# Kernel tuning notes

Measured on AMD Instinct MI355X. Metric: run time of the kernel, lower is better.

Reference implementation:

```python
import jax, jax.numpy as jnp
import numpy as np

EMBED_DIM = 256
UNITS = 512


def setup_inputs() -> dict:
    key = jax.random.key(0)
    k1, k2, k3, k4, k5, k6, k7, k8 = jax.random.split(key, 8)
    B, L = 2048, 64
    features = jax.random.normal(k1, (B, L, EMBED_DIM), dtype=jnp.float32)
    hidden = jax.random.normal(k2, (B, UNITS), dtype=jnp.float32)
    s1 = 1.0 / np.sqrt(EMBED_DIM)
    s2 = 1.0 / np.sqrt(UNITS)
    W1 = jax.random.normal(k3, (EMBED_DIM, UNITS), dtype=jnp.float32) * s1
    b1 = jnp.zeros((UNITS,), dtype=jnp.float32)
    W2 = jax.random.normal(k4, (UNITS, UNITS), dtype=jnp.float32) * s2
    b2 = jnp.zeros((UNITS,), dtype=jnp.float32)
    V = jax.random.normal(k5, (UNITS, 1), dtype=jnp.float32) * s2
    bV = jnp.zeros((1,), dtype=jnp.float32)
    return {"features": features, "hidden": hidden, "W1": W1, "b1": b1,
            "W2": W2, "b2": b2, "V": V, "bV": bV}


def reference(features, hidden, W1, b1, W2, b2, V, bV):
    # features: [B, L, D_feat]; hidden: [B, U]
    # score = tanh(W1(features) + W2(hidden)[:, None])  -> [B, L, U]
    proj_f = jnp.einsum('bld,du->blu', features, W1) + b1
    proj_h = hidden @ W2 + b2                         # [B, U]
    score = jnp.tanh(proj_f + proj_h[:, None, :])     # [B, L, U]
    logits = jnp.einsum('blu,uo->blo', score, V) + bV  # [B, L, 1]
    attention_weights = jax.nn.softmax(logits, axis=1)  # softmax over L
    context_vector = jnp.sum(attention_weights * features, axis=1)  # [B, D_feat]
    return context_vector, attention_weights
```

## Files before the change

### kernel.cpp

```cpp
#include <hip/hip_runtime.h>
#include <math.h>

#define B_N 2048
#define L_N 64
#define D_N 256
#define U_N 512
#define NB  4

typedef __attribute__((ext_vector_type(8))) short bf16x8;
typedef __attribute__((ext_vector_type(4))) float f32x4;

__device__ __forceinline__ float fast_tanh(float x) {
    float e = __builtin_amdgcn_exp2f(x * 2.8853900817779268f);
    float r = __builtin_amdgcn_rcpf(e + 1.0f);
    return fmaf(-2.0f, r, 1.0f);
}
__device__ __forceinline__ ushort f2bf(float x) {
    uint b = __float_as_uint(x);
    uint r = (b + 0x7FFF + ((b >> 16) & 1)) >> 16;
    return (ushort)r;
}
__device__ __forceinline__ float bf2f(ushort u) {
    uint v = ((uint)u) << 16;
    return __uint_as_float(v);
}

__global__ __launch_bounds__(256) void pack_weights(
    const float* __restrict__ W1, const float* __restrict__ W2,
    ushort* __restrict__ W1p, ushort* __restrict__ W2p)
{
    ushort tmp[8];
    if (blockIdx.x < 64) {
        int g = blockIdx.x * 256 + threadIdx.x;
        int ntg = g >> 9, ks = (g >> 6) & 7, lane = g & 63;
        int n  = ntg * 16 + (lane & 15);
        int kb = ks * 32 + (lane >> 4) * 8;
#pragma unroll
        for (int j = 0; j < 8; ++j) tmp[j] = f2bf(W1[(kb + j) * U_N + n]);
        *(uint4*)&W1p[(size_t)g * 8] = *(uint4*)tmp;
    } else {
        int g = (blockIdx.x - 64) * 256 + threadIdx.x;
        int ntg = g >> 10, ks = (g >> 6) & 15, lane = g & 63;
        int n  = ntg * 16 + (lane & 15);
        int kb = ks * 32 + (lane >> 4) * 8;
#pragma unroll
        for (int j = 0; j < 8; ++j) tmp[j] = f2bf(W2[(kb + j) * U_N + n]);
        *(uint4*)&W2p[(size_t)g * 8] = *(uint4*)tmp;
    }
}

__global__ __launch_bounds__(256) void proj_h_mfma(
    const float* __restrict__ hidden, const ushort* __restrict__ W2p,
    const float* __restrict__ b1, const float* __restrict__ b2,
    ushort* __restrict__ ph)
{
    __shared__ ushort As[16 * 512];

    const int t  = threadIdx.x;
    const int b0 = blockIdx.x * 16;
    const int u0 = blockIdx.y * 128;

#pragma unroll
    for (int i = 0; i < 4; ++i) {
        int f = t + i * 256;
        int m = f >> 6, c = f & 63;
        float4 x0 = *(const float4*)&hidden[(b0 + m) * U_N + c * 8];
        float4 x1 = *(const float4*)&hidden[(b0 + m) * U_N + c * 8 + 4];
        ushort tmp[8] = {f2bf(x0.x), f2bf(x0.y), f2bf(x0.z), f2bf(x0.w),
                         f2bf(x1.x), f2bf(x1.y), f2bf(x1.z), f2bf(x1.w)};
        *(uint4*)&As[(m * 64 + (c ^ (m & 7))) * 8] = *(uint4*)tmp;
    }
    __syncthreads();

    const int w = t >> 6, lane = t & 63;
    const int ml = lane & 15, q = lane >> 4;

    f32x4 acc[2];
#pragma unroll
    for (int nt = 0; nt < 2; ++nt) acc[nt] = (f32x4){0.f, 0.f, 0.f, 0.f};

    for (int ks = 0; ks < 16; ++ks) {
        int c = ks * 4 + q;
        bf16x8 a = *(const bf16x8*)&As[(ml * 64 + (c ^ (ml & 7))) * 8];
        bf16x8 bb[2];
#pragma unroll
        for (int nt = 0; nt < 2; ++nt) {
            int ntg = blockIdx.y * 8 + w * 2 + nt;
            bb[nt] = *(const bf16x8*)&W2p[(size_t)((ntg * 16 + ks) * 64 + lane) * 8];
        }
#pragma unroll
        for (int nt = 0; nt < 2; ++nt)
            acc[nt] = __builtin_amdgcn_mfma_f32_16x16x32_bf16(a, bb[nt], acc[nt], 0, 0, 0);
    }

#pragma unroll
    for (int nt = 0; nt < 2; ++nt) {
        int n = u0 + (w * 2 + nt) * 16 + ml;
        float bias = b1[n] + b2[n];
#pragma unroll
        for (int r = 0; r < 4; ++r)
            ph[(size_t)(b0 + q * 4 + r) * U_N + n] = f2bf(acc[nt][r] + bias);
    }
}

__global__ __launch_bounds__(256, 2) void attn_kernel(
    const float* __restrict__ features, const ushort* __restrict__ W1p,
    const float* __restrict__ V, const float* __restrict__ bV,
    const ushort* __restrict__ ph, float* __restrict__ out)
{
    __shared__ ushort As[2][64 * 256];
    __shared__ float lpart[4][64];
    __shared__ float wls[64];

    const int t    = threadIdx.x;
    const int w    = t >> 6;
    const int lane = t & 63;
    const int ml   = lane & 15;
    const int q    = lane >> 4;
    const int b0   = blockIdx.x * NB;

    float4 pf[16];

#define ISSUE(bb) do {                                                        \
        const float* fb_ = features + (size_t)(bb) * (L_N * D_N);             \
        _Pragma("unroll")                                                     \
        for (int i = 0; i < 8; ++i) {                                         \
            int f_ = t + i * 256;                                             \
            int m_ = f_ >> 5, c_ = f_ & 31;                                   \
            pf[2*i]   = *(const float4*)&fb_[m_ * D_N + c_ * 8];              \
            pf[2*i+1] = *(const float4*)&fb_[m_ * D_N + c_ * 8 + 4];          \
        }                                                                     \
    } while (0)

#define WRITE(buf) do {                                                       \
        _Pragma("unroll")                                                     \
        for (int i = 0; i < 8; ++i) {                                         \
            int f_ = t + i * 256;                                             \
            int m_ = f_ >> 5, c_ = f_ & 31;                                   \
            float4 x0_ = pf[2*i], x1_ = pf[2*i+1];                            \
            ushort tmp_[8] = {f2bf(x0_.x), f2bf(x0_.y), f2bf(x0_.z), f2bf(x0_.w), \
                              f2bf(x1_.x), f2bf(x1_.y), f2bf(x1_.z), f2bf(x1_.w)}; \
            *(uint4*)&As[buf][(m_ * 32 + (c_ ^ (m_ & 31))) * 8] = *(uint4*)tmp_;  \
        }                                                                     \
    } while (0)

    ISSUE(b0);
    WRITE(0);
    __syncthreads();

    const ushort* W1w = W1p + (size_t)(w * 8) * 8 * 64 * 8;
    int cur = 0;

    for (int bi = 0; bi < NB; ++bi) {
        const int b = b0 + bi;

        if (bi + 1 < NB) ISSUE(b + 1);
        __builtin_amdgcn_sched_barrier(0);

        float lp[16];
#pragma unroll
        for (int j = 0; j < 16; ++j) lp[j] = 0.f;

        for (int uc = 0; uc < 4; ++uc) {
            f32x4 acc[4][2];
#pragma unroll
            for (int mt = 0; mt < 4; ++mt)
#pragma unroll
                for (int nt = 0; nt < 2; ++nt)
                    acc[mt][nt] = (f32x4){0.f, 0.f, 0.f, 0.f};

            bf16x8 bf0[2], bf1[2], bfn[2];
#pragma unroll
            for (int nt = 0; nt < 2; ++nt) {
                bf0[nt] = *(const bf16x8*)&W1w[(size_t)(((uc * 2 + nt) * 8 + 0) * 64 + lane) * 8];
                bf1[nt] = *(const bf16x8*)&W1w[(size_t)(((uc * 2 + nt) * 8 + 1) * 64 + lane) * 8];
            }

            for (int ks = 0; ks < 8; ++ks) {
                if (ks < 6) {
#pragma unroll
                    for (int nt = 0; nt < 2; ++nt)
                        bfn[nt] = *(const bf16x8*)&W1w[(size_t)(((uc * 2 + nt) * 8 + ks + 2) * 64 + lane) * 8];
                }
                bf16x8 a[4];
#pragma unroll
                for (int mt = 0; mt < 4; ++mt) {
                    int m = mt * 16 + ml;
                    int c = ks * 4 + q;
                    a[mt] = *(const bf16x8*)&As[cur][(m * 32 + (c ^ (m & 31))) * 8];
                }
#pragma unroll
                for (int nt = 0; nt < 2; ++nt)
#pragma unroll
                    for (int mt = 0; mt < 4; ++mt)
                        acc[mt][nt] = __builtin_amdgcn_mfma_f32_16x16x32_bf16(
                            a[mt], bf0[nt], acc[mt][nt], 0, 0, 0);
                bf0[0] = bf1[0]; bf0[1] = bf1[1];
                bf1[0] = bfn[0]; bf1[1] = bfn[1];
            }

#pragma unroll
            for (int nt = 0; nt < 2; ++nt) {
                int n = w * 128 + uc * 32 + nt * 16 + ml;
                float phv = bf2f(ph[(size_t)b * U_N + n]);
                float vv  = V[n];
#pragma unroll
                for (int mt = 0; mt < 4; ++mt)
#pragma unroll
                    for (int r = 0; r < 4; ++r) {
                        float s = fast_tanh(acc[mt][nt][r] + phv);
                        lp[mt * 4 + r] = fmaf(s, vv, lp[mt * 4 + r]);
                    }
            }
        }

#pragma unroll
        for (int off = 1; off <= 8; off <<= 1)
#pragma unroll
            for (int j = 0; j < 16; ++j)
                lp[j] += __shfl_xor(lp[j], off);

        __syncthreads();
        if (bi + 1 < NB) WRITE(cur ^ 1);

        if (ml == 0) {
#pragma unroll
            for (int mt = 0; mt < 4; ++mt)
#pragma unroll
                for (int r = 0; r < 4; ++r)
                    lpart[w][mt * 16 + q * 4 + r] = lp[mt * 4 + r];
        }
        __syncthreads();

        if (t < 64) {
            float lsum = bV[0] + lpart[0][t] + lpart[1][t] + lpart[2][t] + lpart[3][t];
            float mx = lsum;
#pragma unroll
            for (int off = 32; off > 0; off >>= 1)
                mx = fmaxf(mx, __shfl_xor(mx, off));
            float e = __expf(lsum - mx);
            float ssum = e;
#pragma unroll
            for (int off = 32; off > 0; off >>= 1)
                ssum += __shfl_xor(ssum, off);
            float wt = e / ssum;
            wls[t] = wt;
            out[(size_t)B_N * D_N + (size_t)b * L_N + t] = wt;
        }
        __syncthreads();

        float ctx = 0.f;
#pragma unroll 16
        for (int l = 0; l < L_N; ++l) {
            ushort u = As[cur][(l * 32 + ((t >> 3) ^ (l & 31))) * 8 + (t & 7)];
            ctx = fmaf(wls[l], bf2f(u), ctx);
        }
        out[(size_t)b * D_N + t] = ctx;

        cur ^= 1;
    }
#undef ISSUE
#undef WRITE
}

extern "C" void kernel_launch(void* const* d_in, const int* in_sizes, int n_in,
                              void* d_out, int out_size, void* d_ws, size_t ws_size,
                              hipStream_t stream) {
    const float* features = (const float*)d_in[0];
    const float* hidden   = (const float*)d_in[1];
    const float* W1       = (const float*)d_in[2];
    const float* b1       = (const float*)d_in[3];
    const float* W2       = (const float*)d_in[4];
    const float* b2       = (const float*)d_in[5];
    const float* V        = (const float*)d_in[6];
    const float* bV       = (const float*)d_in[7];
    float* out = (float*)d_out;

    ushort* ph  = (ushort*)d_ws;
    ushort* W1p = (ushort*)((char*)d_ws + (size_t)B_N * U_N * 2);
    ushort* W2p = (ushort*)((char*)d_ws + (size_t)B_N * U_N * 2 + (size_t)D_N * U_N * 2);

    pack_weights<<<192, 256, 0, stream>>>(W1, W2, W1p, W2p);
    proj_h_mfma<<<dim3(B_N / 16, U_N / 128), 256, 0, stream>>>(hidden, W2p, b1, b2, ph);
    attn_kernel<<<B_N / NB, 256, 0, stream>>>(features, W1p, V, bV, ph, out);
}
```

Measured before the change: 307.1 us.

## Use 512-thread blocks with split prefetch interleaved into MFMA k-steps

Doubles the block to 512 threads (8 waves) and 8 batches per block. Each wave now covers 64 units over all k-steps rather than looping over 128 units in chunks. The next batch's features load is split into two halves, interleaved between the k-step halves to overlap global loads with MFMA and cut prefetch register pressure. The LDS swizzle moves to the global read address, and the context reduction is split across two thread halves with a shared-memory combine. Costs include an extra barrier per batch and less contiguous global reads.

```diff
diff --git a/kernel.cpp b/kernel.cpp
--- a/kernel.cpp
+++ b/kernel.cpp
@@ -5,7 +5,7 @@
 #define L_N 64
 #define D_N 256
 #define U_N 512
-#define NB  4
+#define NB  8
 
 typedef __attribute__((ext_vector_type(8))) short bf16x8;
 typedef __attribute__((ext_vector_type(4))) float f32x4;
@@ -103,13 +103,14 @@
     }
 }
 
-__global__ __launch_bounds__(256, 2) void attn_kernel(
+__global__ __launch_bounds__(512) void attn_kernel(
     const float* __restrict__ features, const ushort* __restrict__ W1p,
     const float* __restrict__ V, const float* __restrict__ bV,
     const ushort* __restrict__ ph, float* __restrict__ out)
 {
     __shared__ ushort As[2][64 * 256];
-    __shared__ float lpart[4][64];
+    __shared__ float lpart[8][64];
+    __shared__ float ctxp[2][256];
     __shared__ float wls[64];
 
     const int t    = threadIdx.x;
@@ -119,99 +120,106 @@
     const int q    = lane >> 4;
     const int b0   = blockIdx.x * NB;
 
-    float4 pf[16];
-
-#define ISSUE(bb) do {                                                        \
+    float4 pa0, pa1, pb0, pb1;
+
+#define ISSUE_HALF(bb, i0) do {                                               \
         const float* fb_ = features + (size_t)(bb) * (L_N * D_N);             \
+        { int ch_ = t + (i0) * 512; int m_ = ch_ >> 5, cc_ = ch_ & 31;        \
+          const float* s_ = &fb_[m_ * D_N + (cc_ ^ (m_ & 31)) * 8];           \
+          pa0 = *(const float4*)s_; pa1 = *(const float4*)(s_ + 4); }         \
+        { int ch_ = t + (i0 + 1) * 512; int m_ = ch_ >> 5, cc_ = ch_ & 31;    \
+          const float* s_ = &fb_[m_ * D_N + (cc_ ^ (m_ & 31)) * 8];           \
+          pb0 = *(const float4*)s_; pb1 = *(const float4*)(s_ + 4); }         \
+    } while (0)
+
+#define WRITE_HALF(buf, i0) do {                                              \
+        { int ch_ = t + (i0) * 512; int m_ = ch_ >> 5, cc_ = ch_ & 31;        \
+          ushort tv_[8] = {f2bf(pa0.x), f2bf(pa0.y), f2bf(pa0.z), f2bf(pa0.w),\
+                           f2bf(pa1.x), f2bf(pa1.y), f2bf(pa1.z), f2bf(pa1.w)};\
+          *(uint4*)&As[buf][((m_ * 32 + cc_)) * 8] = *(uint4*)tv_; }          \
+        { int ch_ = t + (i0 + 1) * 512; int m_ = ch_ >> 5, cc_ = ch_ & 31;    \
+          ushort tv_[8] = {f2bf(pb0.x), f2bf(pb0.y), f2bf(pb0.z), f2bf(pb0.w),\
+                           f2bf(pb1.x), f2bf(pb1.y), f2bf(pb1.z), f2bf(pb1.w)};\
+          *(uint4*)&As[buf][((m_ * 32 + cc_)) * 8] = *(uint4*)tv_; }          \
+    } while (0)
+
+#define KSTEP(ks) do {                                                        \
+        if ((ks) < 7) {                                                       \
+            _Pragma("unroll")                                                 \
+            for (int nt = 0; nt < 4; ++nt)                                    \
+                bfn[nt] = *(const bf16x8*)&W1w[(size_t)((nt * 8 + (ks) + 1) * 64 + lane) * 8]; \
+        }                                                                     \
+        bf16x8 a_[4];                                                         \
         _Pragma("unroll")                                                     \
-        for (int i = 0; i < 8; ++i) {                                         \
-            int f_ = t + i * 256;                                             \
-            int m_ = f_ >> 5, c_ = f_ & 31;                                   \
-            pf[2*i]   = *(const float4*)&fb_[m_ * D_N + c_ * 8];              \
-            pf[2*i+1] = *(const float4*)&fb_[m_ * D_N + c_ * 8 + 4];          \
+        for (int mt = 0; mt < 4; ++mt) {                                      \
+            int m_ = mt * 16 + ml, c_ = (ks) * 4 + q;                         \
+            a_[mt] = *(const bf16x8*)&As[cur][(m_ * 32 + (c_ ^ (m_ & 31))) * 8]; \
+        }                                                                     \
+        _Pragma("unroll")                                                     \
+        for (int nt = 0; nt < 4; ++nt)                                        \
+            _Pragma("unroll")                                                 \
+            for (int mt = 0; mt < 4; ++mt)                                    \
+                acc[mt][nt] = __builtin_amdgcn_mfma_f32_16x16x32_bf16(        \
+                    a_[mt], bfc[nt], acc[mt][nt], 0, 0, 0);                   \
+        if ((ks) < 7) {                                                       \
+            _Pragma("unroll")                                                 \
+            for (int nt = 0; nt < 4; ++nt) bfc[nt] = bfn[nt];                 \
         }                                                                     \
     } while (0)
 
-#define WRITE(buf) do {                                                       \
-        _Pragma("unroll")                                                     \
-        for (int i = 0; i < 8; ++i) {                                         \
-            int f_ = t + i * 256;                                             \
-            int m_ = f_ >> 5, c_ = f_ & 31;                                   \
-            float4 x0_ = pf[2*i], x1_ = pf[2*i+1];                            \
-            ushort tmp_[8] = {f2bf(x0_.x), f2bf(x0_.y), f2bf(x0_.z), f2bf(x0_.w), \
-                              f2bf(x1_.x), f2bf(x1_.y), f2bf(x1_.z), f2bf(x1_.w)}; \
-            *(uint4*)&As[buf][(m_ * 32 + (c_ ^ (m_ & 31))) * 8] = *(uint4*)tmp_;  \
-        }                                                                     \
-    } while (0)
-
-    ISSUE(b0);
-    WRITE(0);
+    ISSUE_HALF(b0, 0);
+    WRITE_HALF(0, 0);
+    ISSUE_HALF(b0, 2);
+    WRITE_HALF(0, 2);
     __syncthreads();
 
-    const ushort* W1w = W1p + (size_t)(w * 8) * 8 * 64 * 8;
+    const ushort* W1w = W1p + (size_t)(w * 4) * 8 * 64 * 8;
     int cur = 0;
 
     for (int bi = 0; bi < NB; ++bi) {
         const int b = b0 + bi;
-
-        if (bi + 1 < NB) ISSUE(b + 1);
+        const bool pre = (bi + 1 < NB);
+
+        if (pre) ISSUE_HALF(b + 1, 0);
         __builtin_amdgcn_sched_barrier(0);
 
+        f32x4 acc[4][4];
+#pragma unroll
+        for (int mt = 0; mt < 4; ++mt)
+#pragma unroll
+            for (int nt = 0; nt < 4; ++nt)
+                acc[mt][nt] = (f32x4){0.f, 0.f, 0.f, 0.f};
+
+        bf16x8 bfc[4], bfn[4];
+#pragma unroll
+        for (int nt = 0; nt < 4; ++nt)
+            bfc[nt] = *(const bf16x8*)&W1w[(size_t)((nt * 8) * 64 + lane) * 8];
+
+        KSTEP(0); KSTEP(1); KSTEP(2); KSTEP(3);
+
+        if (pre) {
+            WRITE_HALF(cur ^ 1, 0);
+            ISSUE_HALF(b + 1, 2);
+        }
+        __builtin_amdgcn_sched_barrier(0);
+
+        KSTEP(4); KSTEP(5); KSTEP(6); KSTEP(7);
+
         float lp[16];
 #pragma unroll
         for (int j = 0; j < 16; ++j) lp[j] = 0.f;
-
-        for (int uc = 0; uc < 4; ++uc) {
-            f32x4 acc[4][2];
+#pragma unroll
+        for (int nt = 0; nt < 4; ++nt) {
+            int n = w * 64 + nt * 16 + ml;
+            float phv = bf2f(ph[(size_t)b * U_N + n]);
+            float vv  = V[n];
 #pragma unroll
             for (int mt = 0; mt < 4; ++mt)
 #pragma unroll
-                for (int nt = 0; nt < 2; ++nt)
-                    acc[mt][nt] = (f32x4){0.f, 0.f, 0.f, 0.f};
-
-            bf16x8 bf0[2], bf1[2], bfn[2];
-#pragma unroll
-            for (int nt = 0; nt < 2; ++nt) {
-                bf0[nt] = *(const bf16x8*)&W1w[(size_t)(((uc * 2 + nt) * 8 + 0) * 64 + lane) * 8];
-                bf1[nt] = *(const bf16x8*)&W1w[(size_t)(((uc * 2 + nt) * 8 + 1) * 64 + lane) * 8];
-            }
-
-            for (int ks = 0; ks < 8; ++ks) {
-                if (ks < 6) {
-#pragma unroll
-                    for (int nt = 0; nt < 2; ++nt)
-                        bfn[nt] = *(const bf16x8*)&W1w[(size_t)(((uc * 2 + nt) * 8 + ks + 2) * 64 + lane) * 8];
+                for (int r = 0; r < 4; ++r) {
+                    float s = fast_tanh(acc[mt][nt][r] + phv);
+                    lp[mt * 4 + r] = fmaf(s, vv, lp[mt * 4 + r]);
                 }
-                bf16x8 a[4];
-#pragma unroll
-                for (int mt = 0; mt < 4; ++mt) {
-                    int m = mt * 16 + ml;
-                    int c = ks * 4 + q;
-                    a[mt] = *(const bf16x8*)&As[cur][(m * 32 + (c ^ (m & 31))) * 8];
-                }
-#pragma unroll
-                for (int nt = 0; nt < 2; ++nt)
-#pragma unroll
-                    for (int mt = 0; mt < 4; ++mt)
-                        acc[mt][nt] = __builtin_amdgcn_mfma_f32_16x16x32_bf16(
-                            a[mt], bf0[nt], acc[mt][nt], 0, 0, 0);
-                bf0[0] = bf1[0]; bf0[1] = bf1[1];
-                bf1[0] = bfn[0]; bf1[1] = bfn[1];
-            }
-
-#pragma unroll
-            for (int nt = 0; nt < 2; ++nt) {
-                int n = w * 128 + uc * 32 + nt * 16 + ml;
-                float phv = bf2f(ph[(size_t)b * U_N + n]);
-                float vv  = V[n];
-#pragma unroll
-                for (int mt = 0; mt < 4; ++mt)
-#pragma unroll
-                    for (int r = 0; r < 4; ++r) {
-                        float s = fast_tanh(acc[mt][nt][r] + phv);
-                        lp[mt * 4 + r] = fmaf(s, vv, lp[mt * 4 + r]);
-                    }
-            }
         }
 
 #pragma unroll
@@ -220,8 +228,7 @@
             for (int j = 0; j < 16; ++j)
                 lp[j] += __shfl_xor(lp[j], off);
 
-        __syncthreads();
-        if (bi + 1 < NB) WRITE(cur ^ 1);
+        if (pre) WRITE_HALF(cur ^ 1, 2);
 
         if (ml == 0) {
 #pragma unroll
@@ -233,7 +240,9 @@
         __syncthreads();
 
         if (t < 64) {
-            float lsum = bV[0] + lpart[0][t] + lpart[1][t] + lpart[2][t] + lpart[3][t];
+            float lsum = bV[0];
+#pragma unroll
+            for (int ww = 0; ww < 8; ++ww) lsum += lpart[ww][t];
             float mx = lsum;
 #pragma unroll
             for (int off = 32; off > 0; off >>= 1)
@@ -249,18 +258,26 @@
         }
         __syncthreads();
 
-        float ctx = 0.f;
-#pragma unroll 16
-        for (int l = 0; l < L_N; ++l) {
-            ushort u = As[cur][(l * 32 + ((t >> 3) ^ (l & 31))) * 8 + (t & 7)];
-            ctx = fmaf(wls[l], bf2f(u), ctx);
-        }
-        out[(size_t)b * D_N + t] = ctx;
+        {
+            int d = t & 255, h = t >> 8;
+            float cx = 0.f;
+#pragma unroll 8
+            for (int li = 0; li < 32; ++li) {
+                int l = h * 32 + li;
+                ushort u = As[cur][(l * 32 + ((d >> 3) ^ (l & 31))) * 8 + (d & 7)];
+                cx = fmaf(wls[l], bf2f(u), cx);
+            }
+            ctxp[h][d] = cx;
+        }
+        __syncthreads();
+
+        if (t < 256) out[(size_t)b * D_N + t] = ctxp[0][t] + ctxp[1][t];
 
         cur ^= 1;
     }
-#undef ISSUE
-#undef WRITE
+#undef ISSUE_HALF
+#undef WRITE_HALF
+#undef KSTEP
 }
 
 extern "C" void kernel_launch(void* const* d_in, const int* in_sizes, int n_in,
@@ -282,5 +299,5 @@
 
     pack_weights<<<192, 256, 0, stream>>>(W1, W2, W1p, W2p);
     proj_h_mfma<<<dim3(B_N / 16, U_N / 128), 256, 0, stream>>>(hidden, W2p, b1, b2, ph);
-    attn_kernel<<<B_N / NB, 256, 0, stream>>>(features, W1p, V, bV, ph, out);
-}
+    attn_kernel<<<B_N / NB, 512, 0, stream>>>(features, W1p, V, bV, ph, out);
+}
```

Result: no change. 303.4 us (-1.2%).
